# Performance work log

Hardware: AMD Instinct MI355X
Metric: run time of the kernel (lower is better)

## Reference

```python
import jax, jax.numpy as jnp
from jax import lax
import numpy as np

DIM = 384
HEADS = 8
SR = 2
B, D0, D1, D2 = 4, 16, 16, 16
N = 1 + D0 * D1 * D2


def setup_inputs() -> dict:
    key = jax.random.key(0)
    ks = jax.random.split(key, 8)
    s = 0.02
    return {
        "x": jax.random.normal(ks[0], (B, N, DIM), dtype=jnp.float32),
        "q_w": jax.random.normal(ks[1], (DIM, DIM), dtype=jnp.float32) * s,
        "kv_w": jax.random.normal(ks[2], (2 * DIM, DIM), dtype=jnp.float32) * s,
        "proj_w": jax.random.normal(ks[3], (DIM, DIM), dtype=jnp.float32) * s,
        "proj_b": jnp.zeros((DIM,), dtype=jnp.float32),
        "sr_w": jax.random.normal(ks[4], (DIM, 1, SR, SR, SR), dtype=jnp.float32) * s,  # depthwise (groups=dim)
        "sr_b": jnp.zeros((DIM,), dtype=jnp.float32),
        "ln_g": jnp.ones((DIM,), dtype=jnp.float32),
        "ln_b": jnp.zeros((DIM,), dtype=jnp.float32),
        "d0": D0, "d1": D1, "d2": D2,
    }


def reference(x, q_w, kv_w, proj_w, proj_b, sr_w, sr_b, ln_g, ln_b, d0, d1, d2):
    B_, N_, C = x.shape
    hd = C // HEADS
    scale = hd ** -0.5

    # q projection -> [B, H, N, hd]
    q = (x @ q_w.T).reshape(B_, N_, HEADS, hd).transpose(0, 2, 1, 3)

    # spatial reduction of patch tokens (keep CLS token)
    x_ = x[:, 1:].transpose(0, 2, 1).reshape(B_, C, d0, d1, d2)
    x_ = lax.conv_general_dilated(
        x_, sr_w, window_strides=(SR, SR, SR), padding="VALID",
        dimension_numbers=("NCDHW", "OIDHW", "NCDHW"), feature_group_count=C,
    ) + sr_b[None, :, None, None, None]
    x_ = x_.reshape(B_, C, -1).transpose(0, 2, 1)           # [B, M-1, C]
    x_ = jnp.concatenate([x[:, 0:1], x_], axis=1)            # [B, M, C]

    # LayerNorm (eps=1e-5)
    mu = jnp.mean(x_, axis=-1, keepdims=True)
    var = jnp.var(x_, axis=-1, keepdims=True)
    x_ = (x_ - mu) / jnp.sqrt(var + 1e-5) * ln_g + ln_b

    M = x_.shape[1]
    kv = (x_ @ kv_w.T).reshape(B_, M, 2, HEADS, hd).transpose(2, 0, 3, 1, 4)
    k, v = kv[0], kv[1]                                      # [B, H, M, hd]

    attn = jax.nn.softmax(jnp.einsum("bhnd,bhmd->bhnm", q, k) * scale, axis=-1)
    out = jnp.einsum("bhnm,bhmd->bhnd", attn, v)
    out = out.transpose(0, 2, 1, 3).reshape(B_, N_, C)
    return out @ proj_w.T + proj_b
```

## Files before the change

### kernel.cpp

```cpp
#include <hip/hip_runtime.h>

typedef unsigned short u16;
typedef unsigned int u32;
typedef __bf16 bf16x8 __attribute__((ext_vector_type(8)));
typedef float f32x4 __attribute__((ext_vector_type(4)));

#define NTOK 4097
#define MTOK 513
#define MPAD 544
#define KPAD 640
#define NPAD_Q 4224
#define ROWS_X 16512

__device__ __forceinline__ u16 f2bf(float f) {
  u32 u = __builtin_bit_cast(u32, f);
  u = u + 0x7FFFu + ((u >> 16) & 1u);
  return (u16)(u >> 16);
}
__device__ __forceinline__ u16 f2bf_fast(float f) {
  u32 u = __builtin_bit_cast(u32, f);
  return (u16)((u + 0x8000u) >> 16);
}

__device__ __forceinline__ void gld16(const u16* g, u16* l) {
  __builtin_amdgcn_global_load_lds((const __attribute__((address_space(1))) u32*)g,
                                   (__attribute__((address_space(3))) u32*)l, 16, 0, 0);
}

#define NQW  147456
#define NKVW 294912
#define NPW  147456
#define GQW  (NQW / 8)
#define GKVW (NKVW / 8)
#define GPW  (NPW / 8)
#define SRLN_BLOCKS (4 * MTOK)

__global__ void wcast_kernel(const float* __restrict__ qw, const float* __restrict__ kvw,
                             const float* __restrict__ pw, u16* __restrict__ qwb,
                             u16* __restrict__ kvwb, u16* __restrict__ pwb) {
  const int GW = GQW + GKVW + GPW;
  int idx = blockIdx.x * blockDim.x + threadIdx.x;
  int stride = gridDim.x * blockDim.x;
  for (int g = idx; g < GW; g += stride) {
    const float* s;
    u16* d;
    int off;
    if (g < GQW) { s = qw; d = qwb; off = g * 8; }
    else if (g < GQW + GKVW) { s = kvw; d = kvwb; off = (g - GQW) * 8; }
    else { s = pw; d = pwb; off = (g - GQW - GKVW) * 8; }
    float4 v0 = *(const float4*)(s + off);
    float4 v1 = *(const float4*)(s + off + 4);
    uint4 o;
    u16* p = (u16*)&o;
    p[0] = f2bf(v0.x); p[1] = f2bf(v0.y); p[2] = f2bf(v0.z); p[3] = f2bf(v0.w);
    p[4] = f2bf(v1.x); p[5] = f2bf(v1.y); p[6] = f2bf(v1.z); p[7] = f2bf(v1.w);
    *(uint4*)(d + off) = o;
  }
}

__global__ __launch_bounds__(384, 3) void fused_q_srln(
    const float* __restrict__ x, const u16* __restrict__ qwb,
    const float* __restrict__ srw, const float* __restrict__ srb,
    const float* __restrict__ lng, const float* __restrict__ lnb,
    u16* __restrict__ qb, u16* __restrict__ xln) {
  __shared__ __align__(16) u16 aLds[2 * 128 * 64];
  __shared__ __align__(16) u16 bLds[2 * 128 * 64];
  __shared__ float r1[6], r2[6];
  int bx = blockIdx.x;
  if (bx < 387) {
    int tid = threadIdx.x, w = tid >> 6, lane = tid & 63, q4 = lane >> 4, c16 = lane & 15;
    bool act = tid < 256;
    int wr = w >> 1, wc = w & 1;
    int x7 = c16 & 7;
    size_t rbase = (size_t)(bx % 129) * 128;
    int c0 = (bx / 129) * 128;

    float4 ra[4][2];
    auto loadA = [&](int kc) {
#pragma unroll
      for (int i = 0; i < 4; i++) {
        int s = (w * 4 + i) * 64 + lane;
        int row = s >> 3, chp = s & 7;
        int ch = chp ^ (row & 7);
        int ar = (int)rbase + row;
        if (ar > 16387) ar = 16387;
        const float* pa = x + (size_t)ar * 384 + kc * 64 + ch * 8;
        ra[i][0] = *(const float4*)pa;
        ra[i][1] = *(const float4*)(pa + 4);
      }
    };
    auto writeA = [&](int buf) {
#pragma unroll
      for (int i = 0; i < 4; i++) {
        uint4 oa;
        u16* p = (u16*)&oa;
        p[0] = f2bf(ra[i][0].x); p[1] = f2bf(ra[i][0].y);
        p[2] = f2bf(ra[i][0].z); p[3] = f2bf(ra[i][0].w);
        p[4] = f2bf(ra[i][1].x); p[5] = f2bf(ra[i][1].y);
        p[6] = f2bf(ra[i][1].z); p[7] = f2bf(ra[i][1].w);
        *(uint4*)(&aLds[buf * 8192 + (w * 4 + i) * 512 + lane * 8]) = oa;
      }
    };
    auto stageB = [&](int kc, int buf) {
#pragma unroll
      for (int i = 0; i < 4; i++) {
        int s = (w * 4 + i) * 64 + lane;
        int row = s >> 3, chp = s & 7;
        int ch = chp ^ (row & 7);
        gld16(qwb + (size_t)(c0 + row) * 384 + kc * 64 + ch * 8,
              &bLds[buf * 8192 + (w * 4 + i) * 512]);
      }
    };

    if (act) {
      loadA(0);
      stageB(0, 0);
      writeA(0);
    }
    __syncthreads();

    f32x4 acc[4][4];
#pragma unroll
    for (int mt = 0; mt < 4; mt++)
#pragma unroll
      for (int nt = 0; nt < 4; nt++) acc[mt][nt] = (f32x4){0, 0, 0, 0};

    for (int c = 0; c < 6; c++) {
      int cb = c & 1, nb = cb ^ 1;
      if (act && c < 5) {
        loadA(c + 1);
        stageB(c + 1, nb);
      }
      if (act) {
#pragma unroll
        for (int ks = 0; ks < 2; ks++) {
          bf16x8 af[4], bf[4];
#pragma unroll
          for (int mt = 0; mt < 4; mt++)
            af[mt] = *(const bf16x8*)(&aLds[cb * 8192 + (wr * 64 + mt * 16 + c16) * 64 + ((ks * 4 + q4) ^ x7) * 8]);
#pragma unroll
          for (int nt = 0; nt < 4; nt++)
            bf[nt] = *(const bf16x8*)(&bLds[cb * 8192 + (wc * 64 + nt * 16 + c16) * 64 + ((ks * 4 + q4) ^ x7) * 8]);
#pragma unroll
          for (int mt = 0; mt < 4; mt++)
#pragma unroll
            for (int nt = 0; nt < 4; nt++)
              acc[mt][nt] = __builtin_amdgcn_mfma_f32_16x16x32_bf16(af[mt], bf[nt], acc[mt][nt], 0, 0, 0);
        }
      }
      if (act && c < 5) writeA(nb);
      __syncthreads();
    }

    if (act) {
#pragma unroll
      for (int mt = 0; mt < 4; mt++)
#pragma unroll
        for (int nt = 0; nt < 4; nt++) {
          int col = c0 + wc * 64 + nt * 16 + c16;
#pragma unroll
          for (int r = 0; r < 4; r++) {
            int R = (int)rbase + wr * 64 + mt * 16 + q4 * 4 + r;
            int b = R / NTOK;
            if (b >= 4) continue;
            int n = R - b * NTOK;
            int h = col / 48, d = col - h * 48;
            qb[((size_t)(b * 8 + h) * NPAD_Q + n) * 64 + d] =
                f2bf(acc[mt][nt][r] * 0.14433756729740643f);
          }
        }
    }
  } else {
    int c = threadIdx.x;
    int bm = bx - 387;
    int b = bm / MTOK, m = bm - b * MTOK;
    float v;
    if (m == 0) {
      v = x[(b * NTOK) * 384 + c];
    } else {
      int mo = m - 1;
      int oz = mo >> 6, oy = (mo >> 3) & 7, ox = mo & 7;
      float acc = srb[c];
#pragma unroll
      for (int dz = 0; dz < 2; dz++)
#pragma unroll
        for (int dy = 0; dy < 2; dy++)
#pragma unroll
          for (int dx = 0; dx < 2; dx++) {
            int tok = 1 + ((2 * oz + dz) * 256 + (2 * oy + dy) * 16 + (2 * ox + dx));
            acc += x[(b * NTOK + tok) * 384 + c] * srw[c * 8 + dz * 4 + dy * 2 + dx];
          }
      v = acc;
    }
    float s1 = v, s2 = v * v;
#pragma unroll
    for (int msk = 32; msk >= 1; msk >>= 1) {
      s1 += __shfl_xor(s1, msk);
      s2 += __shfl_xor(s2, msk);
    }
    int w = threadIdx.x >> 6, lane = threadIdx.x & 63;
    if (lane == 0) { r1[w] = s1; r2[w] = s2; }
    __syncthreads();
    float S1 = 0.f, S2 = 0.f;
#pragma unroll
    for (int i = 0; i < 6; i++) { S1 += r1[i]; S2 += r2[i]; }
    float mu = S1 * (1.0f / 384.0f);
    float var = S2 * (1.0f / 384.0f) - mu * mu;
    float y = (v - mu) * rsqrtf(var + 1e-5f) * lng[c] + lnb[c];
    xln[(b * MPAD + m) * 384 + c] = f2bf(y);
  }
}

__device__ __forceinline__ void gemm_core(u16* aLds, u16* bLds,
                                          const u16* __restrict__ A, const u16* __restrict__ W,
                                          int mode, size_t rbase, int c0,
                                          u16* __restrict__ o1, u16* __restrict__ o2,
                                          float* __restrict__ of, const float* __restrict__ bias) {
  int tid = threadIdx.x, w = tid >> 6, lane = tid & 63, q4 = lane >> 4, c16 = lane & 15;
  int wr = w >> 1, wc = w & 1;
  int x7 = c16 & 7;

  auto stageAB = [&](int kc, int buf) {
#pragma unroll
    for (int i = 0; i < 4; i++) {
      int s = (w * 4 + i) * 64 + lane;
      int row = s >> 3, chp = s & 7;
      int ch = chp ^ (row & 7);
      gld16(A + (rbase + row) * 384 + kc * 64 + ch * 8, &aLds[buf * 8192 + (w * 4 + i) * 512]);
    }
#pragma unroll
    for (int i = 0; i < 4; i++) {
      int s = (w * 4 + i) * 64 + lane;
      int row = s >> 3, chp = s & 7;
      int ch = chp ^ (row & 7);
      gld16(W + (size_t)(c0 + row) * 384 + kc * 64 + ch * 8, &bLds[buf * 8192 + (w * 4 + i) * 512]);
    }
  };
  stageAB(0, 0);
  __syncthreads();

  f32x4 acc[4][4];
#pragma unroll
  for (int mt = 0; mt < 4; mt++)
#pragma unroll
    for (int nt = 0; nt < 4; nt++) acc[mt][nt] = (f32x4){0, 0, 0, 0};

  for (int c = 0; c < 6; c++) {
    int cb = c & 1, nb = cb ^ 1;
    if (c < 5) stageAB(c + 1, nb);
#pragma unroll
    for (int ks = 0; ks < 2; ks++) {
      bf16x8 af[4], bf[4];
#pragma unroll
      for (int mt = 0; mt < 4; mt++)
        af[mt] = *(const bf16x8*)(&aLds[cb * 8192 + (wr * 64 + mt * 16 + c16) * 64 + ((ks * 4 + q4) ^ x7) * 8]);
#pragma unroll
      for (int nt = 0; nt < 4; nt++)
        bf[nt] = *(const bf16x8*)(&bLds[cb * 8192 + (wc * 64 + nt * 16 + c16) * 64 + ((ks * 4 + q4) ^ x7) * 8]);
#pragma unroll
      for (int mt = 0; mt < 4; mt++)
#pragma unroll
        for (int nt = 0; nt < 4; nt++)
          acc[mt][nt] = __builtin_amdgcn_mfma_f32_16x16x32_bf16(af[mt], bf[nt], acc[mt][nt], 0, 0, 0);
    }
    __syncthreads();
  }

#pragma unroll
  for (int mt = 0; mt < 4; mt++)
#pragma unroll
    for (int nt = 0; nt < 4; nt++) {
      int col = c0 + wc * 64 + nt * 16 + c16;
#pragma unroll
      for (int r = 0; r < 4; r++) {
        int R = (int)rbase + wr * 64 + mt * 16 + q4 * 4 + r;
        float val = acc[mt][nt][r];
        if (mode == 0) {
          int b = R / NTOK;
          if (b >= 4) continue;
          int n = R - b * NTOK;
          int h = col / 48, d = col - h * 48;
          o1[((size_t)(b * 8 + h) * NPAD_Q + n) * 64 + d] = f2bf(val * 0.14433756729740643f);
        } else if (mode == 1) {
          int b = R / MPAD;
          int m = R - b * MPAD;
          if (col < 384) {
            int h = col / 48, d = col - h * 48;
            o1[((size_t)(b * 8 + h) * KPAD + m) * 64 + d] = f2bf(val);
          } else {
            int c2 = col - 384;
            int h = c2 / 48, d = c2 - h * 48;
            o2[((size_t)(b * 8 + h) * 48 + d) * KPAD + m] = f2bf(val);
          }
        } else {
          if (R < 4 * NTOK) of[(size_t)R * 384 + col] = val + bias[col];
        }
      }
    }
}

__global__ __launch_bounds__(256) void gemm_kv(const u16* __restrict__ xlnb, const u16* __restrict__ kvwb,
                                               u16* __restrict__ kb2, u16* __restrict__ vtb) {
  __shared__ __align__(16) u16 aLds[2 * 128 * 64];
  __shared__ __align__(16) u16 bLds[2 * 128 * 64];
  int i = blockIdx.x;
  gemm_core(aLds, bLds, xlnb, kvwb, 1, (size_t)(i % 17) * 128, (i / 17) * 128,
            kb2, vtb, nullptr, nullptr);
}

__global__ __launch_bounds__(256) void gemm_out(const u16* __restrict__ A, const u16* __restrict__ W,
                                                float* __restrict__ of, const float* __restrict__ bias) {
  __shared__ __align__(16) u16 aLds[2 * 128 * 64];
  __shared__ __align__(16) u16 bLds[2 * 128 * 64];
  gemm_core(aLds, bLds, A, W, 2, (size_t)blockIdx.x * 128, blockIdx.y * 128,
            nullptr, nullptr, of, bias);
}

__global__ __launch_bounds__(256, 4) void attn_kernel(const u16* __restrict__ qb,
                                                      const u16* __restrict__ kb,
                                                      const u16* __restrict__ vt,
                                                      u16* __restrict__ outb) {
  __shared__ __align__(16) u16 klds[2][64][64];
  __shared__ __align__(16) u16 vlds[2][48][64];
  __shared__ __align__(16) u16 plds[4][16][76];
  int tid = threadIdx.x, w = tid >> 6, lane = tid & 63, q4 = lane >> 4, c16 = lane & 15;
  int bh = blockIdx.x;
  int n0 = blockIdx.y * 128 + w * 32;
  int r7 = c16 & 7;

  const uint4* qp = (const uint4*)(qb + ((size_t)bh * NPAD_Q + n0 + c16) * 64);
  bf16x8 aq[2][2];
#pragma unroll
  for (int rg = 0; rg < 2; rg++) {
    aq[rg][0] = __builtin_bit_cast(bf16x8, qp[rg * 128 + q4]);
    aq[rg][1] = __builtin_bit_cast(bf16x8, qp[rg * 128 + 4 + q4]);
  }

  const u16* kbase = kb + (size_t)bh * KPAD * 64;
  const u16* vbase = vt + (size_t)bh * 48 * KPAD;

  auto stage = [&](int cn, int buf) {
#pragma unroll
    for (int i = 0; i < 2; i++) {
      int s = (w * 2 + i) * 64 + lane;
      int row = s >> 3, chp = s & 7;
      int ch = chp ^ (row & 7);
      gld16(kbase + (size_t)(cn * 64 + row) * 64 + ch * 8, &klds[buf][(w * 2 + i) * 8][0]);
    }
#pragma unroll
    for (int i = 0; i < 2; i++) {
      int blk = w * 2 + i;
      if (blk < 6) {
        int s = blk * 64 + lane;
        int row = s >> 3, chp = s & 7;
        int ch = chp ^ (row & 7);
        gld16(vbase + (size_t)row * KPAD + cn * 64 + ch * 8, &vlds[buf][blk * 8][0]);
      }
    }
  };

  stage(0, 0);
  __syncthreads();

  f32x4 o[2][3];
  float lsum[2][4];
#pragma unroll
  for (int rg = 0; rg < 2; rg++) {
#pragma unroll
    for (int nt = 0; nt < 3; nt++) o[rg][nt] = (f32x4){0, 0, 0, 0};
#pragma unroll
    for (int r = 0; r < 4; r++) lsum[rg][r] = 0.f;
  }

  for (int c = 0; c < 8; c++) {
    int cb = c & 1, nb = cb ^ 1;
    stage(c + 1, nb);

    f32x4 s[2][4];
#pragma unroll
    for (int rg = 0; rg < 2; rg++)
#pragma unroll
      for (int t = 0; t < 4; t++) s[rg][t] = (f32x4){0, 0, 0, 0};
#pragma unroll
    for (int t = 0; t < 4; t++) {
      const u16* krow = &klds[cb][t * 16 + c16][0];
      bf16x8 k0 = *(const bf16x8*)(krow + (q4 ^ r7) * 8);
      bf16x8 k1 = *(const bf16x8*)(krow + ((q4 ^ r7) ^ 4) * 8);
#pragma unroll
      for (int rg = 0; rg < 2; rg++) {
        s[rg][t] = __builtin_amdgcn_mfma_f32_16x16x32_bf16(aq[rg][0], k0, s[rg][t], 0, 0, 0);
        s[rg][t] = __builtin_amdgcn_mfma_f32_16x16x32_bf16(aq[rg][1], k1, s[rg][t], 0, 0, 0);
      }
    }
#pragma unroll
    for (int rg = 0; rg < 2; rg++)
#pragma unroll
      for (int t = 0; t < 4; t++)
#pragma unroll
        for (int r = 0; r < 4; r++) {
          float e = __expf(s[rg][t][r]);
          s[rg][t][r] = e;
          lsum[rg][r] += e;
        }
    bf16x8 afrag[2][2];
#pragma unroll
    for (int rg = 0; rg < 2; rg++) {
#pragma unroll
      for (int t = 0; t < 4; t++)
#pragma unroll
        for (int r = 0; r < 4; r++) plds[w][q4 * 4 + r][t * 16 + c16] = f2bf_fast(s[rg][t][r]);
#pragma unroll
      for (int kl = 0; kl < 2; kl++)
        afrag[rg][kl] = *(const bf16x8*)(&plds[w][c16][kl * 32 + q4 * 8]);
    }
#pragma unroll
    for (int kl = 0; kl < 2; kl++)
#pragma unroll
      for (int nt = 0; nt < 3; nt++) {
        const u16* vrow = &vlds[cb][nt * 16 + c16][0];
        bf16x8 bv = *(const bf16x8*)(vrow + ((kl * 4 + q4) ^ r7) * 8);
#pragma unroll
        for (int rg = 0; rg < 2; rg++)
          o[rg][nt] = __builtin_amdgcn_mfma_f32_16x16x32_bf16(afrag[rg][kl], bv, o[rg][nt], 0, 0, 0);
      }
    __syncthreads();
  }

  {
    f32x4 s4[2] = {{0, 0, 0, 0}, {0, 0, 0, 0}};
    const u16* krow = &klds[0][c16][0];
    bf16x8 k0 = *(const bf16x8*)(krow + (q4 ^ r7) * 8);
    bf16x8 k1 = *(const bf16x8*)(krow + ((q4 ^ r7) ^ 4) * 8);
#pragma unroll
    for (int rg = 0; rg < 2; rg++) {
      s4[rg] = __builtin_amdgcn_mfma_f32_16x16x32_bf16(aq[rg][0], k0, s4[rg], 0, 0, 0);
      s4[rg] = __builtin_amdgcn_mfma_f32_16x16x32_bf16(aq[rg][1], k1, s4[rg], 0, 0, 0);
    }
    bf16x8 afrag[2];
#pragma unroll
    for (int rg = 0; rg < 2; rg++) {
#pragma unroll
      for (int r = 0; r < 4; r++) {
        float e = (c16 == 0) ? __expf(s4[rg][r]) : 0.f;
        lsum[rg][r] += e;
        plds[w][q4 * 4 + r][c16] = f2bf_fast(e);
        plds[w][q4 * 4 + r][16 + c16] = 0;
      }
      afrag[rg] = *(const bf16x8*)(&plds[w][c16][q4 * 8]);
    }
#pragma unroll
    for (int nt = 0; nt < 3; nt++) {
      const u16* vrow = &vlds[0][nt * 16 + c16][0];
      bf16x8 bv = *(const bf16x8*)(vrow + (q4 ^ r7) * 8);
#pragma unroll
      for (int rg = 0; rg < 2; rg++)
        o[rg][nt] = __builtin_amdgcn_mfma_f32_16x16x32_bf16(afrag[rg], bv, o[rg][nt], 0, 0, 0);
    }
  }

  int b = bh >> 3, h = bh & 7;
#pragma unroll
  for (int rg = 0; rg < 2; rg++) {
    float inv[4];
#pragma unroll
    for (int r = 0; r < 4; r++) {
      float l = lsum[rg][r];
      l += __shfl_xor(l, 1);
      l += __shfl_xor(l, 2);
      l += __shfl_xor(l, 4);
      l += __shfl_xor(l, 8);
      inv[r] = 1.0f / l;
    }
#pragma unroll
    for (int nt = 0; nt < 3; nt++)
#pragma unroll
      for (int r = 0; r < 4; r++) {
        int n = n0 + rg * 16 + q4 * 4 + r;
        if (n < NTOK) outb[((size_t)(b * NTOK + n)) * 384 + h * 48 + nt * 16 + c16] = f2bf(o[rg][nt][r] * inv[r]);
      }
  }
}

extern "C" void kernel_launch(void* const* d_in, const int* in_sizes, int n_in,
                              void* d_out, int out_size, void* d_ws, size_t ws_size,
                              hipStream_t stream) {
  const float* x = (const float*)d_in[0];
  const float* q_w = (const float*)d_in[1];
  const float* kv_w = (const float*)d_in[2];
  const float* proj_w = (const float*)d_in[3];
  const float* proj_b = (const float*)d_in[4];
  const float* sr_w = (const float*)d_in[5];
  const float* sr_b = (const float*)d_in[6];
  const float* ln_g = (const float*)d_in[7];
  const float* ln_b = (const float*)d_in[8];
  float* out = (float*)d_out;

  u16* ws = (u16*)d_ws;
  u16* x_b = ws;
  u16* qw_b = x_b + (size_t)ROWS_X * 384;
  u16* kvw_b = qw_b + 147456;
  u16* pw_b = kvw_b + 294912;
  u16* q_b = pw_b + 147456;
  u16* xln_b = q_b + (size_t)32 * NPAD_Q * 64;
  u16* k_b = xln_b + (size_t)4 * MPAD * 384;
  u16* vt_b = k_b + (size_t)32 * KPAD * 64;
  u16* attn_b = x_b;


  wcast_kernel<<<288, 256, 0, stream>>>(q_w, kv_w, proj_w, qw_b, kvw_b, pw_b);
  fused_q_srln<<<387 + SRLN_BLOCKS, 384, 0, stream>>>(x, qw_b, sr_w, sr_b, ln_g, ln_b, q_b, xln_b);
  gemm_kv<<<102, 256, 0, stream>>>(xln_b, kvw_b, k_b, vt_b);
  attn_kernel<<<dim3(32, 33), 256, 0, stream>>>(q_b, k_b, vt_b, attn_b);
  gemm_out<<<dim3(129, 3), 256, 0, stream>>>(attn_b, pw_b, out, proj_b);
}
```

Baseline: 195.5 us.

## Regroup kernels: fuse weight cast with SR-LN, merge Q and KV GEMMs

The weight-cast kernel now runs inside the spatial-reduction/LayerNorm kernel as extra blocks, and the Q projection GEMM moves out of that kernel into a combined Q+KV GEMM launch using 256-thread blocks. This goes from three launches to two ahead of attention. The Q GEMM no longer has idle threads in 384-wide blocks, and its fp32 A-tile loads are split into halves to lower register pressure. In exchange, the Q GEMM can no longer overlap with the SR-LN work.

```diff
diff --git a/kernel.cpp b/kernel.cpp
--- a/kernel.cpp
+++ b/kernel.cpp
@@ -33,146 +33,19 @@
 #define GQW  (NQW / 8)
 #define GKVW (NKVW / 8)
 #define GPW  (NPW / 8)
+#define GW   (GQW + GKVW + GPW)
 #define SRLN_BLOCKS (4 * MTOK)
-
-__global__ void wcast_kernel(const float* __restrict__ qw, const float* __restrict__ kvw,
-                             const float* __restrict__ pw, u16* __restrict__ qwb,
-                             u16* __restrict__ kvwb, u16* __restrict__ pwb) {
-  const int GW = GQW + GKVW + GPW;
-  int idx = blockIdx.x * blockDim.x + threadIdx.x;
-  int stride = gridDim.x * blockDim.x;
-  for (int g = idx; g < GW; g += stride) {
-    const float* s;
-    u16* d;
-    int off;
-    if (g < GQW) { s = qw; d = qwb; off = g * 8; }
-    else if (g < GQW + GKVW) { s = kvw; d = kvwb; off = (g - GQW) * 8; }
-    else { s = pw; d = pwb; off = (g - GQW - GKVW) * 8; }
-    float4 v0 = *(const float4*)(s + off);
-    float4 v1 = *(const float4*)(s + off + 4);
-    uint4 o;
-    u16* p = (u16*)&o;
-    p[0] = f2bf(v0.x); p[1] = f2bf(v0.y); p[2] = f2bf(v0.z); p[3] = f2bf(v0.w);
-    p[4] = f2bf(v1.x); p[5] = f2bf(v1.y); p[6] = f2bf(v1.z); p[7] = f2bf(v1.w);
-    *(uint4*)(d + off) = o;
-  }
-}
-
-__global__ __launch_bounds__(384, 3) void fused_q_srln(
-    const float* __restrict__ x, const u16* __restrict__ qwb,
-    const float* __restrict__ srw, const float* __restrict__ srb,
-    const float* __restrict__ lng, const float* __restrict__ lnb,
-    u16* __restrict__ qb, u16* __restrict__ xln) {
-  __shared__ __align__(16) u16 aLds[2 * 128 * 64];
-  __shared__ __align__(16) u16 bLds[2 * 128 * 64];
-  __shared__ float r1[6], r2[6];
-  int bx = blockIdx.x;
-  if (bx < 387) {
-    int tid = threadIdx.x, w = tid >> 6, lane = tid & 63, q4 = lane >> 4, c16 = lane & 15;
-    bool act = tid < 256;
-    int wr = w >> 1, wc = w & 1;
-    int x7 = c16 & 7;
-    size_t rbase = (size_t)(bx % 129) * 128;
-    int c0 = (bx / 129) * 128;
-
-    float4 ra[4][2];
-    auto loadA = [&](int kc) {
-#pragma unroll
-      for (int i = 0; i < 4; i++) {
-        int s = (w * 4 + i) * 64 + lane;
-        int row = s >> 3, chp = s & 7;
-        int ch = chp ^ (row & 7);
-        int ar = (int)rbase + row;
-        if (ar > 16387) ar = 16387;
-        const float* pa = x + (size_t)ar * 384 + kc * 64 + ch * 8;
-        ra[i][0] = *(const float4*)pa;
-        ra[i][1] = *(const float4*)(pa + 4);
-      }
-    };
-    auto writeA = [&](int buf) {
-#pragma unroll
-      for (int i = 0; i < 4; i++) {
-        uint4 oa;
-        u16* p = (u16*)&oa;
-        p[0] = f2bf(ra[i][0].x); p[1] = f2bf(ra[i][0].y);
-        p[2] = f2bf(ra[i][0].z); p[3] = f2bf(ra[i][0].w);
-        p[4] = f2bf(ra[i][1].x); p[5] = f2bf(ra[i][1].y);
-        p[6] = f2bf(ra[i][1].z); p[7] = f2bf(ra[i][1].w);
-        *(uint4*)(&aLds[buf * 8192 + (w * 4 + i) * 512 + lane * 8]) = oa;
-      }
-    };
-    auto stageB = [&](int kc, int buf) {
-#pragma unroll
-      for (int i = 0; i < 4; i++) {
-        int s = (w * 4 + i) * 64 + lane;
-        int row = s >> 3, chp = s & 7;
-        int ch = chp ^ (row & 7);
-        gld16(qwb + (size_t)(c0 + row) * 384 + kc * 64 + ch * 8,
-              &bLds[buf * 8192 + (w * 4 + i) * 512]);
-      }
-    };
-
-    if (act) {
-      loadA(0);
-      stageB(0, 0);
-      writeA(0);
-    }
-    __syncthreads();
-
-    f32x4 acc[4][4];
-#pragma unroll
-    for (int mt = 0; mt < 4; mt++)
-#pragma unroll
-      for (int nt = 0; nt < 4; nt++) acc[mt][nt] = (f32x4){0, 0, 0, 0};
-
-    for (int c = 0; c < 6; c++) {
-      int cb = c & 1, nb = cb ^ 1;
-      if (act && c < 5) {
-        loadA(c + 1);
-        stageB(c + 1, nb);
-      }
-      if (act) {
-#pragma unroll
-        for (int ks = 0; ks < 2; ks++) {
-          bf16x8 af[4], bf[4];
-#pragma unroll
-          for (int mt = 0; mt < 4; mt++)
-            af[mt] = *(const bf16x8*)(&aLds[cb * 8192 + (wr * 64 + mt * 16 + c16) * 64 + ((ks * 4 + q4) ^ x7) * 8]);
-#pragma unroll
-          for (int nt = 0; nt < 4; nt++)
-            bf[nt] = *(const bf16x8*)(&bLds[cb * 8192 + (wc * 64 + nt * 16 + c16) * 64 + ((ks * 4 + q4) ^ x7) * 8]);
-#pragma unroll
-          for (int mt = 0; mt < 4; mt++)
-#pragma unroll
-            for (int nt = 0; nt < 4; nt++)
-              acc[mt][nt] = __builtin_amdgcn_mfma_f32_16x16x32_bf16(af[mt], bf[nt], acc[mt][nt], 0, 0, 0);
-        }
-      }
-      if (act && c < 5) writeA(nb);
-      __syncthreads();
-    }
-
-    if (act) {
-#pragma unroll
-      for (int mt = 0; mt < 4; mt++)
-#pragma unroll
-        for (int nt = 0; nt < 4; nt++) {
-          int col = c0 + wc * 64 + nt * 16 + c16;
-#pragma unroll
-          for (int r = 0; r < 4; r++) {
-            int R = (int)rbase + wr * 64 + mt * 16 + q4 * 4 + r;
-            int b = R / NTOK;
-            if (b >= 4) continue;
-            int n = R - b * NTOK;
-            int h = col / 48, d = col - h * 48;
-            qb[((size_t)(b * 8 + h) * NPAD_Q + n) * 64 + d] =
-                f2bf(acc[mt][nt][r] * 0.14433756729740643f);
-          }
-        }
-    }
-  } else {
+#define CAST_BLOCKS 192
+
+__global__ void pre_kernel(const float* __restrict__ x, const float* __restrict__ qw,
+                           const float* __restrict__ kvw, const float* __restrict__ pw,
+                           const float* __restrict__ srw, const float* __restrict__ srb,
+                           const float* __restrict__ lng, const float* __restrict__ lnb,
+                           u16* __restrict__ qwb, u16* __restrict__ kvwb, u16* __restrict__ pwb,
+                           u16* __restrict__ xln) {
+  if (blockIdx.x < SRLN_BLOCKS) {
     int c = threadIdx.x;
-    int bm = bx - 387;
+    int bm = blockIdx.x;
     int b = bm / MTOK, m = bm - b * MTOK;
     float v;
     if (m == 0) {
@@ -198,6 +71,7 @@
       s1 += __shfl_xor(s1, msk);
       s2 += __shfl_xor(s2, msk);
     }
+    __shared__ float r1[6], r2[6];
     int w = threadIdx.x >> 6, lane = threadIdx.x & 63;
     if (lane == 0) { r1[w] = s1; r2[w] = s2; }
     __syncthreads();
@@ -208,6 +82,24 @@
     float var = S2 * (1.0f / 384.0f) - mu * mu;
     float y = (v - mu) * rsqrtf(var + 1e-5f) * lng[c] + lnb[c];
     xln[(b * MPAD + m) * 384 + c] = f2bf(y);
+  } else {
+    int idx = (blockIdx.x - SRLN_BLOCKS) * blockDim.x + threadIdx.x;
+    int stride = (gridDim.x - SRLN_BLOCKS) * blockDim.x;
+    for (int g = idx; g < GW; g += stride) {
+      const float* s;
+      u16* d;
+      int off;
+      if (g < GQW) { s = qw; d = qwb; off = g * 8; }
+      else if (g < GQW + GKVW) { s = kvw; d = kvwb; off = (g - GQW) * 8; }
+      else { s = pw; d = pwb; off = (g - GQW - GKVW) * 8; }
+      float4 v0 = *(const float4*)(s + off);
+      float4 v1 = *(const float4*)(s + off + 4);
+      uint4 o;
+      u16* p = (u16*)&o;
+      p[0] = f2bf(v0.x); p[1] = f2bf(v0.y); p[2] = f2bf(v0.z); p[3] = f2bf(v0.w);
+      p[4] = f2bf(v1.x); p[5] = f2bf(v1.y); p[6] = f2bf(v1.z); p[7] = f2bf(v1.w);
+      *(uint4*)(d + off) = o;
+    }
   }
 }
 
@@ -275,13 +167,7 @@
       for (int r = 0; r < 4; r++) {
         int R = (int)rbase + wr * 64 + mt * 16 + q4 * 4 + r;
         float val = acc[mt][nt][r];
-        if (mode == 0) {
-          int b = R / NTOK;
-          if (b >= 4) continue;
-          int n = R - b * NTOK;
-          int h = col / 48, d = col - h * 48;
-          o1[((size_t)(b * 8 + h) * NPAD_Q + n) * 64 + d] = f2bf(val * 0.14433756729740643f);
-        } else if (mode == 1) {
+        if (mode == 1) {
           int b = R / MPAD;
           int m = R - b * MPAD;
           if (col < 384) {
@@ -299,13 +185,132 @@
     }
 }
 
-__global__ __launch_bounds__(256) void gemm_kv(const u16* __restrict__ xlnb, const u16* __restrict__ kvwb,
-                                               u16* __restrict__ kb2, u16* __restrict__ vtb) {
+__device__ __forceinline__ void gemm_core_f32A(u16* aLds, u16* bLds,
+                                               const float* __restrict__ X, const u16* __restrict__ W,
+                                               size_t rbase, int c0, u16* __restrict__ o1) {
+  int tid = threadIdx.x, w = tid >> 6, lane = tid & 63, q4 = lane >> 4, c16 = lane & 15;
+  int wr = w >> 1, wc = w & 1;
+  int x7 = c16 & 7;
+
+  float4 ra[2][2];
+  auto loadA2 = [&](int kc, int half) {
+#pragma unroll
+    for (int i = 0; i < 2; i++) {
+      int idx2 = half * 2 + i;
+      int s = (w * 4 + idx2) * 64 + lane;
+      int row = s >> 3, chp = s & 7;
+      int ch = chp ^ (row & 7);
+      int ar = (int)rbase + row;
+      if (ar > 16387) ar = 16387;
+      const float* pa = X + (size_t)ar * 384 + kc * 64 + ch * 8;
+      ra[i][0] = *(const float4*)pa;
+      ra[i][1] = *(const float4*)(pa + 4);
+    }
+  };
+  auto writeA2 = [&](int buf, int half) {
+#pragma unroll
+    for (int i = 0; i < 2; i++) {
+      int idx2 = half * 2 + i;
+      uint4 oa;
+      u16* p = (u16*)&oa;
+      p[0] = f2bf(ra[i][0].x); p[1] = f2bf(ra[i][0].y);
+      p[2] = f2bf(ra[i][0].z); p[3] = f2bf(ra[i][0].w);
+      p[4] = f2bf(ra[i][1].x); p[5] = f2bf(ra[i][1].y);
+      p[6] = f2bf(ra[i][1].z); p[7] = f2bf(ra[i][1].w);
+      *(uint4*)(&aLds[buf * 8192 + (w * 4 + idx2) * 512 + lane * 8]) = oa;
+    }
+  };
+  auto stageB = [&](int kc, int buf) {
+#pragma unroll
+    for (int i = 0; i < 4; i++) {
+      int s = (w * 4 + i) * 64 + lane;
+      int row = s >> 3, chp = s & 7;
+      int ch = chp ^ (row & 7);
+      gld16(W + (size_t)(c0 + row) * 384 + kc * 64 + ch * 8, &bLds[buf * 8192 + (w * 4 + i) * 512]);
+    }
+  };
+
+  loadA2(0, 0);
+  stageB(0, 0);
+  writeA2(0, 0);
+  loadA2(0, 1);
+  writeA2(0, 1);
+  __syncthreads();
+
+  f32x4 acc[4][4];
+#pragma unroll
+  for (int mt = 0; mt < 4; mt++)
+#pragma unroll
+    for (int nt = 0; nt < 4; nt++) acc[mt][nt] = (f32x4){0, 0, 0, 0};
+
+  for (int c = 0; c < 6; c++) {
+    int cb = c & 1, nb = cb ^ 1;
+    if (c < 5) { loadA2(c + 1, 0); stageB(c + 1, nb); }
+    {
+      bf16x8 af[4], bf[4];
+#pragma unroll
+      for (int mt = 0; mt < 4; mt++)
+        af[mt] = *(const bf16x8*)(&aLds[cb * 8192 + (wr * 64 + mt * 16 + c16) * 64 + ((0 + q4) ^ x7) * 8]);
+#pragma unroll
+      for (int nt = 0; nt < 4; nt++)
+        bf[nt] = *(const bf16x8*)(&bLds[cb * 8192 + (wc * 64 + nt * 16 + c16) * 64 + ((0 + q4) ^ x7) * 8]);
+#pragma unroll
+      for (int mt = 0; mt < 4; mt++)
+#pragma unroll
+        for (int nt = 0; nt < 4; nt++)
+          acc[mt][nt] = __builtin_amdgcn_mfma_f32_16x16x32_bf16(af[mt], bf[nt], acc[mt][nt], 0, 0, 0);
+    }
+    if (c < 5) { writeA2(nb, 0); loadA2(c + 1, 1); }
+    {
+      bf16x8 af[4], bf[4];
+#pragma unroll
+      for (int mt = 0; mt < 4; mt++)
+        af[mt] = *(const bf16x8*)(&aLds[cb * 8192 + (wr * 64 + mt * 16 + c16) * 64 + ((4 + q4) ^ x7) * 8]);
+#pragma unroll
+      for (int nt = 0; nt < 4; nt++)
+        bf[nt] = *(const bf16x8*)(&bLds[cb * 8192 + (wc * 64 + nt * 16 + c16) * 64 + ((4 + q4) ^ x7) * 8]);
+#pragma unroll
+      for (int mt = 0; mt < 4; mt++)
+#pragma unroll
+        for (int nt = 0; nt < 4; nt++)
+          acc[mt][nt] = __builtin_amdgcn_mfma_f32_16x16x32_bf16(af[mt], bf[nt], acc[mt][nt], 0, 0, 0);
+    }
+    if (c < 5) writeA2(nb, 1);
+    __syncthreads();
+  }
+
+#pragma unroll
+  for (int mt = 0; mt < 4; mt++)
+#pragma unroll
+    for (int nt = 0; nt < 4; nt++) {
+      int col = c0 + wc * 64 + nt * 16 + c16;
+#pragma unroll
+      for (int r = 0; r < 4; r++) {
+        int R = (int)rbase + wr * 64 + mt * 16 + q4 * 4 + r;
+        int b = R / NTOK;
+        if (b >= 4) continue;
+        int n = R - b * NTOK;
+        int h = col / 48, d = col - h * 48;
+        o1[((size_t)(b * 8 + h) * NPAD_Q + n) * 64 + d] =
+            f2bf(acc[mt][nt][r] * 0.14433756729740643f);
+      }
+    }
+}
+
+__global__ __launch_bounds__(256) void gemm_qkv(const float* __restrict__ x, const u16* __restrict__ qwb,
+                                                const u16* __restrict__ xlnb, const u16* __restrict__ kvwb,
+                                                u16* __restrict__ qb, u16* __restrict__ kb2,
+                                                u16* __restrict__ vtb) {
   __shared__ __align__(16) u16 aLds[2 * 128 * 64];
   __shared__ __align__(16) u16 bLds[2 * 128 * 64];
-  int i = blockIdx.x;
-  gemm_core(aLds, bLds, xlnb, kvwb, 1, (size_t)(i % 17) * 128, (i / 17) * 128,
-            kb2, vtb, nullptr, nullptr);
+  int bx = blockIdx.x;
+  if (bx < 387) {
+    gemm_core_f32A(aLds, bLds, x, qwb, (size_t)(bx % 129) * 128, (bx / 129) * 128, qb);
+  } else {
+    int i = bx - 387;
+    gemm_core(aLds, bLds, xlnb, kvwb, 1, (size_t)(i % 17) * 128, (i / 17) * 128,
+              kb2, vtb, nullptr, nullptr);
+  }
 }
 
 __global__ __launch_bounds__(256) void gemm_out(const u16* __restrict__ A, const u16* __restrict__ W,
@@ -507,9 +512,9 @@
   u16* attn_b = x_b;
 
 
-  wcast_kernel<<<288, 256, 0, stream>>>(q_w, kv_w, proj_w, qw_b, kvw_b, pw_b);
-  fused_q_srln<<<387 + SRLN_BLOCKS, 384, 0, stream>>>(x, qw_b, sr_w, sr_b, ln_g, ln_b, q_b, xln_b);
-  gemm_kv<<<102, 256, 0, stream>>>(xln_b, kvw_b, k_b, vt_b);
+  pre_kernel<<<SRLN_BLOCKS + CAST_BLOCKS, 384, 0, stream>>>(x, q_w, kv_w, proj_w, sr_w, sr_b,
+                                                            ln_g, ln_b, qw_b, kvw_b, pw_b, xln_b);
+  gemm_qkv<<<489, 256, 0, stream>>>(x, qw_b, xln_b, kvw_b, q_b, k_b, vt_b);
   attn_kernel<<<dim3(32, 33), 256, 0, stream>>>(q_b, k_b, vt_b, attn_b);
   gemm_out<<<dim3(129, 3), 256, 0, stream>>>(attn_b, pw_b, out, proj_b);
 }
```

Measured after the change: 177.3 us. 1.1x faster.
